# Kernel optimization log

Measured on AMD Instinct MI355X. Metric: run time of the kernel, lower is better.

## Reference

```python
import jax, jax.numpy as jnp
import numpy as np
from jax import lax

REP_THR = 0.6
BORDER = 10


def setup_inputs() -> dict:
    key = jax.random.key(0)
    # repeatability heatmap in [0, 1), NCHW
    repeatability = jax.random.uniform(key, (16, 1, 1536, 1536), dtype=jnp.float32)
    return {"repeatability": repeatability}


def _local_max(x):
    # 3x3 stride-1 max pool with padding=1 (torch pads with -inf for maxpool)
    return lax.reduce_window(
        x, -jnp.inf, lax.max,
        window_dimensions=(1, 1, 3, 3),
        window_strides=(1, 1, 1, 1),
        padding=((0, 0), (0, 0), (1, 1), (1, 1)),
    )


def reference(repeatability):
    B, C, H, W = repeatability.shape
    maxima = (repeatability == _local_max(repeatability)) & (repeatability >= REP_THR)
    # border mask: zero out a 10-pixel frame
    border = jnp.zeros((H, W), dtype=bool).at[BORDER:-BORDER, BORDER:-BORDER].set(True)
    maxima = maxima & border  # broadcasts over (B, C)
    # nonzero().t()[2:4] -> row/col (y, x) coordinates of surviving maxima, shape [2, K]
    idx = jnp.nonzero(maxima)  # tuple (b, c, y, x); dynamic-shaped, eager only
    return jnp.stack(idx)[2:4]
```

## Files before the change

kernel.cpp:

```cpp
#include <hip/hip_runtime.h>

#define W 1536
#define H 1536
#define NB 16
#define NROWS (NB * H)
#define SH 16
#define NBLK1 (NROWS / SH)
#define BLOCK1 384
#define CPR 24
#define NMASK (NROWS * CPR)
#define REP_THR 0.6f

__device__ __forceinline__ float max3f(float a, float b, float c) {
    return fmaxf(fmaxf(a, b), c);
}

__device__ __forceinline__ float4 ld4u(const float* p) {
    float4 r;
    __builtin_memcpy(&r, p, 16);
    return r;
}

__global__ __launch_bounds__(BLOCK1) void nms_pass1(const float* __restrict__ in,
                                                    unsigned long long* __restrict__ masks,
                                                    unsigned int* __restrict__ counts) {
    const int t = threadIdx.x;
    const int lane = t & 63;
    const int wv = t >> 6;
    const int blk = blockIdx.x;
    const int r0 = blk * SH;
    const int ytile = blk % (H / SH);

    const int ca = (t == 0) ? 0 : 4 * t - 1;
    const int cb = (t == BLOCK1 - 1) ? 4 * t : 4 * t + 1;

    unsigned colm = 0xFu;
    if (t <= 1) colm = 0u;
    else if (t == 2) colm = 0xCu;
    if (t >= 382) colm = 0u;
    else if (t == 381) colm = 0x3u;

    auto rowp = [&](int i) {
        int ir = r0 - 1 + i;
        ir = ir < 0 ? 0 : (ir >= NROWS ? NROWS - 1 : ir);
        return in + (size_t)ir * W;
    };

    float4 va0 = ld4u(rowp(0) + ca), vb0 = ld4u(rowp(0) + cb);
    float4 va1 = ld4u(rowp(1) + ca), vb1 = ld4u(rowp(1) + cb);
    float4 vaN = ld4u(rowp(2) + ca), vbN = ld4u(rowp(2) + cb);

    float4 hA, hB, ctrB;
    hA.x = max3f(va0.x, va0.y, va0.z);
    hA.y = max3f(va0.y, va0.z, va0.w);
    hA.z = max3f(vb0.x, vb0.y, vb0.z);
    hA.w = max3f(vb0.y, vb0.z, vb0.w);
    hB.x = max3f(va1.x, va1.y, va1.z);
    hB.y = max3f(va1.y, va1.z, va1.w);
    hB.z = max3f(vb1.x, vb1.y, vb1.z);
    hB.w = max3f(vb1.y, vb1.z, vb1.w);
    ctrB.x = va1.y; ctrB.y = va1.z; ctrB.z = va1.w; ctrB.w = vb1.z;

    unsigned cnt = 0;
#pragma unroll
    for (int i = 2; i <= SH + 1; ++i) {
        float4 va = vaN, vb = vbN;
        vaN = ld4u(rowp(i + 1) + ca);
        vbN = ld4u(rowp(i + 1) + cb);
        float4 hC;
        hC.x = max3f(va.x, va.y, va.z);
        hC.y = max3f(va.y, va.z, va.w);
        hC.z = max3f(vb.x, vb.y, vb.z);
        hC.w = max3f(vb.y, vb.z, vb.w);

        const int yloc = ytile * SH + (i - 2);
        unsigned nib = 0u;
        if (yloc >= 10 && yloc < H - 10) {
            nib |= (ctrB.x >= fmaxf(max3f(hA.x, hB.x, hC.x), REP_THR)) ? 1u : 0u;
            nib |= (ctrB.y >= fmaxf(max3f(hA.y, hB.y, hC.y), REP_THR)) ? 2u : 0u;
            nib |= (ctrB.z >= fmaxf(max3f(hA.z, hB.z, hC.z), REP_THR)) ? 4u : 0u;
            nib |= (ctrB.w >= fmaxf(max3f(hA.w, hB.w, hC.w), REP_THR)) ? 8u : 0u;
            nib &= colm;
        }
        cnt += __popc(nib);
        unsigned x = nib;
        x |= __shfl_down(x, 1, 64) << 4;
        x |= __shfl_down(x, 2, 64) << 8;
        x |= __shfl_down(x, 4, 64) << 16;
        unsigned hi = __shfl_down(x, 8, 64);
        if ((lane & 15) == 0) {
            unsigned long long m64 = (unsigned long long)x | ((unsigned long long)hi << 32);
            masks[(size_t)(r0 + i - 2) * CPR + (t >> 4)] = m64;
        }
        hA = hB; hB = hC;
        ctrB.x = va.y; ctrB.y = va.z; ctrB.z = va.w; ctrB.w = vb.z;
    }

#pragma unroll
    for (int o = 32; o > 0; o >>= 1) cnt += __shfl_down(cnt, o, 64);
    __shared__ unsigned wsum[BLOCK1 / 64];
    if (lane == 0) wsum[wv] = cnt;
    __syncthreads();
    if (t == 0) {
        unsigned s = 0;
#pragma unroll
        for (int k = 0; k < BLOCK1 / 64; ++k) s += wsum[k];
        counts[blk] = s;
    }
}

__global__ __launch_bounds__(256) void nms_scan(const unsigned int* __restrict__ counts,
                                                unsigned int* __restrict__ offsets) {
    const int t = threadIdx.x;
    const int lane = t & 63, wv = t >> 6;
    unsigned v[6];
    unsigned sum = 0;
#pragma unroll
    for (int k = 0; k < 6; ++k) { v[k] = counts[t * 6 + k]; sum += v[k]; }
    unsigned incl = sum;
#pragma unroll
    for (int o = 1; o < 64; o <<= 1) {
        unsigned u = __shfl_up(incl, o, 64);
        if (lane >= o) incl += u;
    }
    __shared__ unsigned wtot[4];
    if (lane == 63) wtot[wv] = incl;
    __syncthreads();
    unsigned base = incl - sum;
#pragma unroll
    for (int k = 0; k < 4; ++k) base += (k < wv) ? wtot[k] : 0u;
#pragma unroll
    for (int k = 0; k < 6; ++k) { offsets[t * 6 + k] = base; base += v[k]; }
}

__global__ __launch_bounds__(BLOCK1) void nms_pass3(const unsigned long long* __restrict__ masks,
                                                    const unsigned int* __restrict__ offsets,
                                                    int* __restrict__ out, unsigned int K) {
    const int t = threadIdx.x, lane = t & 63, wv = t >> 6;
    const int blk = blockIdx.x;
    unsigned long long bits = masks[(size_t)blk * (SH * CPR) + t];
    const unsigned cnt = (unsigned)__popcll(bits);
    unsigned incl = cnt;
#pragma unroll
    for (int o = 1; o < 64; o <<= 1) {
        unsigned u = __shfl_up(incl, o, 64);
        if (lane >= o) incl += u;
    }
    __shared__ unsigned wtot[BLOCK1 / 64];
    if (lane == 63) wtot[wv] = incl;
    __syncthreads();
    unsigned wbase = 0;
#pragma unroll
    for (int k = 0; k < BLOCK1 / 64; ++k) wbase += (k < wv) ? wtot[k] : 0u;
    unsigned pos = offsets[blk] + wbase + (incl - cnt);
    if (bits) {
        const int y = (blk % (H / SH)) * SH + t / CPR;
        const int x0 = (t % CPR) * 64;
        while (bits) {
            int j = __builtin_ctzll(bits);
            bits &= bits - 1ull;
            if (pos < K) { out[pos] = y; out[K + pos] = x0 + j; }
            ++pos;
        }
    }
}

extern "C" void kernel_launch(void* const* d_in, const int* in_sizes, int n_in,
                              void* d_out, int out_size, void* d_ws, size_t ws_size,
                              hipStream_t stream) {
    const float* in = (const float*)d_in[0];
    int* out = (int*)d_out;
    unsigned long long* masks = (unsigned long long*)d_ws;
    unsigned int* counts = (unsigned int*)((char*)d_ws + (size_t)NMASK * 8);
    unsigned int* offsets = counts + NBLK1;
    const unsigned K = (unsigned)(out_size / 2);

    nms_pass1<<<NBLK1, BLOCK1, 0, stream>>>(in, masks, counts);
    nms_scan<<<1, 256, 0, stream>>>(counts, offsets);
    nms_pass3<<<NBLK1, BLOCK1, 0, stream>>>(masks, offsets, out, K);
}
```

Before: 245.2 us.

## Fold block-offset scan into scatter kernel and double rows per tile

Removes the separate single-block scan kernel. Each scatter block now computes its global offset by reducing the per-block counts of all earlier blocks directly. The row tile height doubles, which halves the block count, reduces halo row re-reads in the first pass, and lets the scatter block cover a whole tile with 768 threads. The trade-off is redundant prefix work in every scatter block, plus a longer unrolled loop and fewer blocks in the first pass.

New measurement: 252.2 us. 2.9% more time.

```diff
diff --git a/kernel.cpp b/kernel.cpp
--- a/kernel.cpp
+++ b/kernel.cpp
@@ -4,11 +4,12 @@
 #define H 1536
 #define NB 16
 #define NROWS (NB * H)
-#define SH 16
+#define SH 32
 #define NBLK1 (NROWS / SH)
 #define BLOCK1 384
 #define CPR 24
 #define NMASK (NROWS * CPR)
+#define BLOCK2 (SH * CPR)
 #define REP_THR 0.6f
 
 __device__ __forceinline__ float max3f(float a, float b, float c) {
@@ -109,36 +110,12 @@
     }
 }
 
-__global__ __launch_bounds__(256) void nms_scan(const unsigned int* __restrict__ counts,
-                                                unsigned int* __restrict__ offsets) {
-    const int t = threadIdx.x;
-    const int lane = t & 63, wv = t >> 6;
-    unsigned v[6];
-    unsigned sum = 0;
-#pragma unroll
-    for (int k = 0; k < 6; ++k) { v[k] = counts[t * 6 + k]; sum += v[k]; }
-    unsigned incl = sum;
-#pragma unroll
-    for (int o = 1; o < 64; o <<= 1) {
-        unsigned u = __shfl_up(incl, o, 64);
-        if (lane >= o) incl += u;
-    }
-    __shared__ unsigned wtot[4];
-    if (lane == 63) wtot[wv] = incl;
-    __syncthreads();
-    unsigned base = incl - sum;
-#pragma unroll
-    for (int k = 0; k < 4; ++k) base += (k < wv) ? wtot[k] : 0u;
-#pragma unroll
-    for (int k = 0; k < 6; ++k) { offsets[t * 6 + k] = base; base += v[k]; }
-}
-
-__global__ __launch_bounds__(BLOCK1) void nms_pass3(const unsigned long long* __restrict__ masks,
-                                                    const unsigned int* __restrict__ offsets,
-                                                    int* __restrict__ out, unsigned int K) {
+__global__ __launch_bounds__(BLOCK2) void nms_scatter(const unsigned long long* __restrict__ masks,
+                                                      const unsigned int* __restrict__ counts,
+                                                      int* __restrict__ out, unsigned int K) {
     const int t = threadIdx.x, lane = t & 63, wv = t >> 6;
     const int blk = blockIdx.x;
-    unsigned long long bits = masks[(size_t)blk * (SH * CPR) + t];
+    unsigned long long bits = masks[(size_t)blk * BLOCK2 + t];
     const unsigned cnt = (unsigned)__popcll(bits);
     unsigned incl = cnt;
 #pragma unroll
@@ -146,13 +123,20 @@
         unsigned u = __shfl_up(incl, o, 64);
         if (lane >= o) incl += u;
     }
-    __shared__ unsigned wtot[BLOCK1 / 64];
+    unsigned part = (t < blk) ? counts[t] : 0u;
+#pragma unroll
+    for (int o = 32; o > 0; o >>= 1) part += __shfl_down(part, o, 64);
+    __shared__ unsigned wtot[BLOCK2 / 64];
+    __shared__ unsigned coff[BLOCK2 / 64];
     if (lane == 63) wtot[wv] = incl;
+    if (lane == 0) coff[wv] = part;
     __syncthreads();
-    unsigned wbase = 0;
+    unsigned pos = incl - cnt;
 #pragma unroll
-    for (int k = 0; k < BLOCK1 / 64; ++k) wbase += (k < wv) ? wtot[k] : 0u;
-    unsigned pos = offsets[blk] + wbase + (incl - cnt);
+    for (int k = 0; k < BLOCK2 / 64; ++k) {
+        pos += coff[k];
+        pos += (k < wv) ? wtot[k] : 0u;
+    }
     if (bits) {
         const int y = (blk % (H / SH)) * SH + t / CPR;
         const int x0 = (t % CPR) * 64;
@@ -172,10 +156,8 @@
     int* out = (int*)d_out;
     unsigned long long* masks = (unsigned long long*)d_ws;
     unsigned int* counts = (unsigned int*)((char*)d_ws + (size_t)NMASK * 8);
-    unsigned int* offsets = counts + NBLK1;
     const unsigned K = (unsigned)(out_size / 2);
 
     nms_pass1<<<NBLK1, BLOCK1, 0, stream>>>(in, masks, counts);
-    nms_scan<<<1, 256, 0, stream>>>(counts, offsets);
-    nms_pass3<<<NBLK1, BLOCK1, 0, stream>>>(masks, offsets, out, K);
+    nms_scatter<<<NBLK1, BLOCK2, 0, stream>>>(masks, counts, out, K);
 }
```
